# Optimization experiments

Hardware: AMD Instinct MI355X
Metric: run time of the kernel (lower is better)

Reference implementation:

```python
import jax, jax.numpy as jnp
import numpy as np

N = 50000      # nodes
DEG = 32       # avg degree
E = N * DEG + N  # edges incl. self loops
IN_DIM = 512
H = 4          # heads
D = 128        # hidden per head
SLOPE = 0.2


def setup_inputs() -> dict:
    key = jax.random.key(0)
    ks = jax.random.split(key, 12)
    features = jax.random.normal(ks[0], (N, IN_DIM), dtype=jnp.float32)
    src_r = jax.random.randint(ks[1], (N * DEG,), 0, N)
    dst_r = jax.random.randint(ks[2], (N * DEG,), 0, N)
    loop = jnp.arange(N)
    src = jnp.concatenate([src_r, loop]).astype(jnp.int32)
    dst = jnp.concatenate([dst_r, loop]).astype(jnp.int32)
    ids = jax.random.randint(ks[3], (16,), 0, N)
    s0 = 1.0 / np.sqrt(IN_DIM)
    s1 = 1.0 / np.sqrt(H * D)
    fc_w0 = jax.random.normal(ks[4], (IN_DIM, H * D), dtype=jnp.float32) * s0
    attn_l0 = jax.random.normal(ks[5], (H, D), dtype=jnp.float32) * s1
    attn_r0 = jax.random.normal(ks[6], (H, D), dtype=jnp.float32) * s1
    bias0 = jnp.zeros((H * D,), dtype=jnp.float32)
    fc_w1 = jax.random.normal(ks[7], (H * D, H * D), dtype=jnp.float32) * s1
    attn_l1 = jax.random.normal(ks[8], (H, D), dtype=jnp.float32) * s1
    attn_r1 = jax.random.normal(ks[9], (H, D), dtype=jnp.float32) * s1
    bias1 = jnp.zeros((H * D,), dtype=jnp.float32)
    return dict(features=features, fc_w0=fc_w0, attn_l0=attn_l0, attn_r0=attn_r0,
                bias0=bias0, fc_w1=fc_w1, attn_l1=attn_l1, attn_r1=attn_r1,
                bias1=bias1, src=src, dst=dst, ids=ids)


def gat_layer(h, fc_w, attn_l, attn_r, bias, src, dst, residual):
    ft = (h @ fc_w).reshape(N, H, D)                     # [N,H,D]
    el = jnp.sum(ft * attn_l, axis=-1)                   # [N,H]
    er = jnp.sum(ft * attn_r, axis=-1)                   # [N,H]
    e = jax.nn.leaky_relu(el[src] + er[dst], SLOPE)      # [E,H]
    # edge softmax over incoming edges of each dst node (self-loops guarantee coverage)
    emax = jax.ops.segment_max(e, dst, num_segments=N)   # [N,H]
    ee = jnp.exp(e - emax[dst])
    esum = jax.ops.segment_sum(ee, dst, num_segments=N)  # [N,H]
    alpha = ee / esum[dst]                               # [E,H]
    out = jax.ops.segment_sum(alpha[:, :, None] * ft[src], dst, num_segments=N)  # [N,H,D]
    if residual:
        out = out + h.reshape(N, H, D)                   # res_fc is Identity (in == H*D)
    out = out + bias.reshape(1, H, D)
    out = jax.nn.elu(out)
    return out.reshape(N, H * D)


def reference(features, fc_w0, attn_l0, attn_r0, bias0, fc_w1, attn_l1, attn_r1,
              bias1, src, dst, ids):
    h = gat_layer(features, fc_w0, attn_l0, attn_r0, bias0, src, dst, residual=False)
    h = gat_layer(h, fc_w1, attn_l1, attn_r1, bias1, src, dst, residual=True)
    h = jnp.tanh(h)
    return h[ids]  # [B, H*D] gather per id2node lookup
```

## Files before the change

kernel.cpp:

```cpp
#include <hip/hip_runtime.h>
#include <hip/hip_bf16.h>

typedef short bf16x8 __attribute__((ext_vector_type(8)));
typedef float f32x4 __attribute__((ext_vector_type(4)));

#define HD 512
#define KDIM 512
#define NHEAD 4
#define DHEAD 128
#define C1CAP 1024
#define C2CAP 16384
#define E1CAP 2048
#define E2CAP 32768
#define SCATB 64

struct PassSM {
    unsigned bm[1568];
    int2 eBuf[256];
    int fBuf[256];
    int sid[16];
    int eCnt, fCnt, eBase, fBase, s_c;
};

union PrepSM {
    PassSM pass;
    float tile[64][65];
    int s_c;
};

struct GemmSM {
    __hip_bfloat16 As[128][40];
    __hip_bfloat16 Bs[128][40];
    float pel[2][128];
    float perr[2][128];
};

__device__ int detect_bf16(const unsigned short* f, int* s_c) {
    int c = 0;
#pragma unroll
    for (int k = 0; k < 4; ++k) {
        unsigned short u = f[2 * (threadIdx.x + k * 256)];
        int e = (u >> 7) & 0xFF;
        c += (e >= 96 && e <= 140) ? 1 : 0;
    }
#pragma unroll
    for (int off = 32; off; off >>= 1) c += __shfl_xor(c, off, 64);
    if (threadIdx.x == 0) *s_c = 0;
    __syncthreads();
    if ((threadIdx.x & 63) == 0) atomicAdd(s_c, c);
    __syncthreads();
    int r = (*s_c > 512) ? 1 : 0;
    __syncthreads();
    return r;
}

template<int MODE>
__device__ void pass_scan(int pid, const int* __restrict__ src,
                          const int* __restrict__ dst, int E, int B,
                          const int* __restrict__ map1g, PassSM& sm,
                          int2* __restrict__ elist, int* ecnt, int ecap,
                          int* __restrict__ cntArr,
                          int* __restrict__ mapm, int* __restrict__ Flist,
                          int* nFr, int fcap) {
    const int t = threadIdx.x;
    const int nq = E >> 2;
    const int gid = pid * 256 + t;
    if (gid < nq) {
        const int4 d4 = ((const int4*)dst)[gid];
        const int dv[4] = {d4.x, d4.y, d4.z, d4.w};
#pragma unroll
        for (int k = 0; k < 4; ++k) {
            const int d = dv[k];
            if ((sm.bm[d >> 5] >> (d & 31)) & 1u) {
                const int e = 4 * gid + k;
                int slot;
                if (MODE == 0) {
                    slot = 0;
                    for (int q = 0; q < B; ++q) if (sm.sid[q] == d) slot = q;
                } else {
                    slot = map1g[d]; if (slot < 0) slot = 0;
                }
                int p = atomicAdd(&cntArr[slot], 1);
                int2 v; v.x = src[e]; v.y = slot | (p << (MODE == 0 ? 4 : 10));
                int pp = atomicAdd(&sm.eCnt, 1);
                if (pp < 256) sm.eBuf[pp] = v;
                else { int q = atomicAdd(ecnt, 1); if (q < ecap) elist[q] = v; }
                const int s = v.x;
                if (atomicCAS(&mapm[s], -1, -2) == -1) {
                    int q = atomicAdd(&sm.fCnt, 1);
                    if (q < 256) sm.fBuf[q] = s;
                    else {
                        int g2 = atomicAdd(nFr, 1);
                        if (g2 < fcap) { Flist[g2] = s; mapm[s] = g2; }
                        else mapm[s] = 0;
                    }
                }
            }
        }
    }
    __syncthreads();
    const int ne = (sm.eCnt < 256) ? sm.eCnt : 256;
    const int nf = (sm.fCnt < 256) ? sm.fCnt : 256;
    if (t == 0 && ne) sm.eBase = atomicAdd(ecnt, ne);
    if (t == 64 && nf) sm.fBase = atomicAdd(nFr, nf);
    __syncthreads();
    for (int i = t; i < ne; i += 256) {
        int pos = sm.eBase + i;
        if (pos < ecap) elist[pos] = sm.eBuf[i];
    }
    for (int i = t; i < nf; i += 256) {
        int q = sm.fBase + i; int s = sm.fBuf[i];
        if (q < fcap) { Flist[q] = s; mapm[s] = q; }
        else mapm[s] = 0;
    }
}

__device__ void gemm_tile(const __hip_bfloat16* __restrict__ A,
                          const __hip_bfloat16* __restrict__ Bt,
                          __hip_bfloat16* __restrict__ C,
                          const float* __restrict__ al_, const float* __restrict__ ar_,
                          float* __restrict__ el, float* __restrict__ er,
                          int cntv, int m0, int n0, GemmSM& sm) {
    const int t = threadIdx.x;
    const int lane = t & 63, wave = t >> 6;
    const int wm = (wave >> 1) * 64, wn = (wave & 1) * 64;
    const int fr = lane & 15, fk = (lane >> 4) * 8;
    const int r0 = t >> 2;
    const int c0 = (t & 3) * 8;

    int arow[2];
#pragma unroll
    for (int r = 0; r < 2; ++r) {
        int rr = m0 + r * 64 + r0;
        if (rr >= cntv) rr = cntv - 1;
        arow[r] = rr;
    }

    auto loadAB = [&](int kt, uint4 va[2], uint4 vb[2]) {
#pragma unroll
        for (int r = 0; r < 2; ++r) {
            va[r] = *(const uint4*)&A[(size_t)arow[r] * KDIM + kt + c0];
            int row = r * 64 + r0;
            vb[r] = *(const uint4*)&Bt[(size_t)(n0 + row) * KDIM + kt + c0];
        }
    };

    f32x4 acc[4][4];
#pragma unroll
    for (int i = 0; i < 4; ++i)
#pragma unroll
        for (int j = 0; j < 4; ++j)
#pragma unroll
            for (int r = 0; r < 4; ++r) acc[i][j][r] = 0.f;

    uint4 cva[2], cvb[2], nva[2], nvb[2];
    loadAB(0, cva, cvb);
    for (int kt = 0; kt < KDIM; kt += 32) {
#pragma unroll
        for (int r = 0; r < 2; ++r) {
            int row = r * 64 + r0;
            *(uint4*)&sm.As[row][c0] = cva[r];
            *(uint4*)&sm.Bs[row][c0] = cvb[r];
        }
        __syncthreads();
        if (kt + 32 < KDIM) loadAB(kt + 32, nva, nvb);
        bf16x8 af[4], bfr[4];
#pragma unroll
        for (int i = 0; i < 4; ++i) af[i]  = *(const bf16x8*)&sm.As[wm + i * 16 + fr][fk];
#pragma unroll
        for (int j = 0; j < 4; ++j) bfr[j] = *(const bf16x8*)&sm.Bs[wn + j * 16 + fr][fk];
#pragma unroll
        for (int i = 0; i < 4; ++i)
#pragma unroll
            for (int j = 0; j < 4; ++j)
                acc[i][j] = __builtin_amdgcn_mfma_f32_16x16x32_bf16(af[i], bfr[j], acc[i][j], 0, 0, 0);
        __syncthreads();
#pragma unroll
        for (int r = 0; r < 2; ++r) { cva[r] = nva[r]; cvb[r] = nvb[r]; }
    }

    const int cr = (lane >> 4) * 4;
    const int cc = lane & 15;
#pragma unroll
    for (int i = 0; i < 4; ++i)
#pragma unroll
        for (int j = 0; j < 4; ++j)
#pragma unroll
            for (int rg = 0; rg < 4; ++rg) {
                int m = m0 + wm + i * 16 + cr + rg;
                int n = n0 + wn + j * 16 + cc;
                C[(size_t)m * HD + n] = __float2bfloat16(acc[i][j][rg]);
            }

    const int h = n0 >> 7;
    float alv[4], arv[4];
#pragma unroll
    for (int j = 0; j < 4; ++j) {
        alv[j] = al_[h * DHEAD + wn + j * 16 + cc];
        arv[j] = ar_[h * DHEAD + wn + j * 16 + cc];
    }
#pragma unroll
    for (int i = 0; i < 4; ++i)
#pragma unroll
        for (int rg = 0; rg < 4; ++rg) {
            float sl = 0.f, sr = 0.f;
#pragma unroll
            for (int j = 0; j < 4; ++j) {
                float c = acc[i][j][rg];
                sl += c * alv[j];
                sr += c * arv[j];
            }
#pragma unroll
            for (int off = 1; off < 16; off <<= 1) {
                sl += __shfl_xor(sl, off, 16);
                sr += __shfl_xor(sr, off, 16);
            }
            if (cc == 0) {
                int row = wm + i * 16 + cr + rg;
                sm.pel[wn >> 6][row] = sl;
                sm.perr[wn >> 6][row] = sr;
            }
        }
    __syncthreads();
    if (t < 128) {
        int m = m0 + t;
        if (m < cntv) {
            el[m * NHEAD + h] = sm.pel[0][t] + sm.pel[1][t];
            er[m * NHEAD + h] = sm.perr[0][t] + sm.perr[1][t];
        }
    }
    __syncthreads();
}

__global__ __launch_bounds__(256) void prep_pass1_k(
    const void* __restrict__ features,
    const void* __restrict__ W0, const void* __restrict__ W1,
    __hip_bfloat16* __restrict__ Wt0, __hip_bfloat16* __restrict__ Wt1,
    const void* p0, const void* p1, const void* p2,
    const void* p3, const void* p4, const void* p5,
    float* __restrict__ smallc,
    const int* __restrict__ ids, int B, int* __restrict__ mapId,
    const int* __restrict__ src, const int* __restrict__ dst, int E,
    int2* __restrict__ E1l, int* __restrict__ counters,
    int* __restrict__ cnt1, int* __restrict__ map1, int* __restrict__ F1list) {
    __shared__ PrepSM sm;
    const int b = blockIdx.x;
    const int t = threadIdx.x;
    if (b < 128) {
        const int isbf = detect_bf16((const unsigned short*)features, &sm.s_c);
        const int mtx = b >> 6;
        const int tidx = b & 63;
        const int i0 = (tidx >> 3) * 64, j0 = (tidx & 7) * 64;
        const void* W = mtx ? W1 : W0;
        __hip_bfloat16* Wt = mtx ? Wt1 : Wt0;
        const int rr = t >> 6, cc = t & 63;
#pragma unroll
        for (int it = 0; it < 16; ++it) {
            int ii = rr + it * 4;
            size_t idx = (size_t)(i0 + ii) * 512 + j0 + cc;
            float v = isbf ? __bfloat162float(((const __hip_bfloat16*)W)[idx])
                           : ((const float*)W)[idx];
            sm.tile[ii][cc] = v;
        }
        __syncthreads();
#pragma unroll
        for (int it = 0; it < 16; ++it) {
            int jj = rr + it * 4;
            Wt[(size_t)(j0 + jj) * 512 + i0 + cc] = __float2bfloat16(sm.tile[cc][jj]);
        }
    } else if (b < 134) {
        const int isbf = detect_bf16((const unsigned short*)features, &sm.s_c);
        int which = b - 128;
        const void* p;
        switch (which) {
            case 0: p = p0; break;
            case 1: p = p1; break;
            case 2: p = p2; break;
            case 3: p = p3; break;
            case 4: p = p4; break;
            default: p = p5; break;
        }
#pragma unroll
        for (int r = 0; r < 2; ++r) {
            int e = t + r * 256;
            float v = isbf ? __bfloat162float(((const __hip_bfloat16*)p)[e])
                           : ((const float*)p)[e];
            smallc[which * 512 + e] = v;
        }
    } else if (b == 134) {
        if (t < B) atomicMax(&mapId[ids[t]], t);
    } else {
        const int pid = b - 135;
        for (int i = t; i < 1568; i += 256) sm.pass.bm[i] = 0u;
        if (t < 16) sm.pass.sid[t] = (t < B) ? ids[t] : -1;
        if (t == 0) { sm.pass.eCnt = 0; sm.pass.fCnt = 0; }
        __syncthreads();
        if (t < B) { int n = sm.pass.sid[t]; atomicOr(&sm.pass.bm[n >> 5], 1u << (n & 31)); }
        __syncthreads();
        pass_scan<0>(pid, src, dst, E, B, nullptr, sm.pass,
                     E1l, counters + 0, E1CAP, cnt1,
                     map1, F1list, counters + 2, C1CAP);
    }
}

__global__ __launch_bounds__(256) void pass2_k(
    const int* __restrict__ src, const int* __restrict__ dst, int E,
    const int* __restrict__ F1list, int* __restrict__ counters,
    const int* __restrict__ map1,
    int2* __restrict__ E2l, int* __restrict__ cnt2,
    int* __restrict__ map2, int* __restrict__ F2list) {
    __shared__ PassSM sm;
    const int t = threadIdx.x;
    for (int i = t; i < 1568; i += 256) sm.bm[i] = 0u;
    if (t == 0) { sm.eCnt = 0; sm.fCnt = 0; }
    __syncthreads();
    int nf1 = counters[2]; if (nf1 > C1CAP) nf1 = C1CAP;
    for (int i = t; i < nf1; i += 256) {
        int n = F1list[i];
        atomicOr(&sm.bm[n >> 5], 1u << (n & 31));
    }
    __syncthreads();
    pass_scan<1>(blockIdx.x, src, dst, E, 0, map1, sm,
                 E2l, counters + 1, E2CAP, cnt2,
                 map2, F2list, counters + 3, C2CAP);
}

__global__ __launch_bounds__(256) void gathscat_k(
    const void* __restrict__ feat, const int* __restrict__ F2list,
    const int* __restrict__ counters,
    const int* __restrict__ cnt1, const int* __restrict__ cnt2,
    const int2* __restrict__ E1l, const int2* __restrict__ E2l,
    const int* __restrict__ map1, const int* __restrict__ map2,
    int* __restrict__ off1, int* __restrict__ off2,
    int* __restrict__ b1, int* __restrict__ b2,
    __hip_bfloat16* __restrict__ Ac) {
    __shared__ int soff[1024];
    __shared__ int sc[256];
    __shared__ int s1[16];
    __shared__ int s_c;
    const int t = threadIdx.x;
    const int b = blockIdx.x;
    if (b < SCATB) {
        int c0 = cnt2[t * 4 + 0], c1 = cnt2[t * 4 + 1];
        int c2 = cnt2[t * 4 + 2], c3 = cnt2[t * 4 + 3];
        int tsum = c0 + c1 + c2 + c3;
        sc[t] = tsum;
        __syncthreads();
        for (int off = 1; off < 256; off <<= 1) {
            int x = (t >= off) ? sc[t - off] : 0;
            __syncthreads();
            sc[t] += x;
            __syncthreads();
        }
        int run = sc[t] - tsum;
        int b4 = t * 4;
        soff[b4 + 0] = run; run += c0;
        soff[b4 + 1] = run; run += c1;
        soff[b4 + 2] = run; run += c2;
        soff[b4 + 3] = run; run += c3;
        if (t == 0) {
            int acc = 0;
            for (int i = 0; i < 16; ++i) { s1[i] = acc; acc += cnt1[i]; }
            if (b == 0) {
                int a2 = 0;
                for (int i = 0; i < 16; ++i) { off1[i] = a2; a2 += cnt1[i]; }
                off1[16] = a2;
            }
        }
        if (b == 0) {
#pragma unroll
            for (int k = 0; k < 4; ++k) off2[b4 + k] = soff[b4 + k];
            if (t == 255) off2[1024] = run;
        }
        __syncthreads();
        int n2 = counters[1]; if (n2 > E2CAP) n2 = E2CAP;
        for (int i = b * 256 + t; i < n2; i += SCATB * 256) {
            int2 v = E2l[i];
            int y = v.y & 1023, p = v.y >> 10;
            int pos = soff[y] + p;
            int r = map2[v.x]; if (r < 0) r = 0;
            if (pos < E2CAP) b2[pos] = r;
        }
        int n1 = counters[0]; if (n1 > E1CAP) n1 = E1CAP;
        for (int i = b * 256 + t; i < n1; i += SCATB * 256) {
            int2 v = E1l[i];
            int y = v.y & 15, p = v.y >> 4;
            int pos = s1[y] + p;
            int r = map1[v.x]; if (r < 0) r = 0;
            if (pos < E1CAP) b1[pos] = r;
        }
    } else {
        const int isbf = detect_bf16((const unsigned short*)feat, &s_c);
        int cnt = counters[3]; if (cnt > C2CAP) cnt = C2CAP;
        for (int bb = b - SCATB; bb < cnt; bb += (int)gridDim.x - SCATB) {
            int row = F2list[bb];
            __hip_bfloat162 v;
            if (isbf) {
                v = *(const __hip_bfloat162*)&((const __hip_bfloat16*)feat)[(size_t)row * KDIM + t * 2];
            } else {
                const float2 f = *(const float2*)&((const float*)feat)[(size_t)row * KDIM + t * 2];
                v.x = __float2bfloat16(f.x);
                v.y = __float2bfloat16(f.y);
            }
            *(__hip_bfloat162*)&Ac[(size_t)bb * KDIM + t * 2] = v;
        }
    }
}

__global__ __launch_bounds__(256) void gemmel_k(
    const __hip_bfloat16* __restrict__ A,
    const __hip_bfloat16* __restrict__ Bt, __hip_bfloat16* __restrict__ C,
    const float* __restrict__ al_, const float* __restrict__ ar_,
    float* __restrict__ el, float* __restrict__ er,
    const int* __restrict__ countp, int cap) {
    __shared__ alignas(16) GemmSM sm;
    int cntv = *countp; if (cntv > cap) cntv = cap;
    const int nt = ((cntv + 127) >> 7) * 4;
    for (int tile = blockIdx.x; tile < nt; tile += (int)gridDim.x)
        gemm_tile(A, Bt, C, al_, ar_, el, er,
                  cntv, (tile >> 2) * 128, (tile & 3) * 128, sm);
}

__global__ __launch_bounds__(256) void agg1_k(
    const int* __restrict__ off2, const int* __restrict__ b2,
    const int* __restrict__ F1list, const int* __restrict__ map2,
    const int* __restrict__ nF1p,
    const float* __restrict__ el, const float* __restrict__ er,
    const __hip_bfloat16* __restrict__ ftc,
    const float* __restrict__ bias,
    __hip_bfloat16* __restrict__ outc) {
    int b = blockIdx.x;
    if (b >= *nF1p) return;
    int n = F1list[b];
    const int h = threadIdx.x >> 6, lane = threadIdx.x & 63;
    int rn = map2[n]; if (rn < 0) rn = 0;
    float ern = er[rn * NHEAD + h];
    int beg = off2[b], end = off2[b + 1];
    float m = -3.0e38f, l = 0.f, a0 = 0.f, a1 = 0.f;
    int i = beg;
    for (; i + 4 <= end; i += 4) {
        int r4[4]; float ev[4]; __hip_bfloat162 fv[4];
#pragma unroll
        for (int k = 0; k < 4; ++k) {
            int r = b2[i + k]; if ((unsigned)r >= C2CAP) r = 0;
            r4[k] = r;
        }
#pragma unroll
        for (int k = 0; k < 4; ++k) {
            ev[k] = el[r4[k] * NHEAD + h];
            fv[k] = *(const __hip_bfloat162*)&ftc[(size_t)r4[k] * HD + h * DHEAD + lane * 2];
        }
#pragma unroll
        for (int k = 0; k < 4; ++k) {
            float e = ev[k] + ern;
            e = (e >= 0.f) ? e : 0.2f * e;
            float mn = fmaxf(m, e);
            float sc = __expf(m - mn);
            float w  = __expf(e - mn);
            l  = l * sc + w;
            a0 = a0 * sc + w * __bfloat162float(fv[k].x);
            a1 = a1 * sc + w * __bfloat162float(fv[k].y);
            m = mn;
        }
    }
    for (; i < end; ++i) {
        int r2 = b2[i]; if ((unsigned)r2 >= C2CAP) r2 = 0;
        float e = el[r2 * NHEAD + h] + ern;
        e = (e >= 0.f) ? e : 0.2f * e;
        float mn = fmaxf(m, e);
        float sc = __expf(m - mn);
        float w  = __expf(e - mn);
        const __hip_bfloat162 f = *(const __hip_bfloat162*)&ftc[(size_t)r2 * HD + h * DHEAD + lane * 2];
        l  = l * sc + w;
        a0 = a0 * sc + w * __bfloat162float(f.x);
        a1 = a1 * sc + w * __bfloat162float(f.y);
        m = mn;
    }
    float inv = (l > 0.f) ? 1.0f / l : 0.f;
    float o0 = a0 * inv, o1 = a1 * inv;
    const float2 bb = *(const float2*)&bias[h * DHEAD + lane * 2];
    o0 += bb.x; o1 += bb.y;
    o0 = (o0 > 0.f) ? o0 : expm1f(o0);
    o1 = (o1 > 0.f) ? o1 : expm1f(o1);
    __hip_bfloat162 o2;
    o2.x = __float2bfloat16(o0);
    o2.y = __float2bfloat16(o1);
    *(__hip_bfloat162*)&outc[(size_t)b * HD + h * DHEAD + lane * 2] = o2;
}

__global__ __launch_bounds__(256) void agg2_k(
    const int* __restrict__ off1, const int* __restrict__ b1,
    const int* __restrict__ ids, const int* __restrict__ mapId,
    const int* __restrict__ map1,
    const float* __restrict__ el, const float* __restrict__ er,
    const __hip_bfloat16* __restrict__ ftc,
    const __hip_bfloat16* __restrict__ resc,
    const float* __restrict__ bias,
    void* __restrict__ out, const void* __restrict__ features) {
    __shared__ int s_c;
    const int isbf = detect_bf16((const unsigned short*)features, &s_c);
    int b = blockIdx.x;
    int n = ids[b];
    int slot = mapId[n]; if (slot < 0) slot = 0;
    const int h = threadIdx.x >> 6, lane = threadIdx.x & 63;
    int rn = map1[n]; if (rn < 0) rn = 0;
    float ern = er[rn * NHEAD + h];
    int beg = off1[slot], end = off1[slot + 1];
    float m = -3.0e38f, l = 0.f, a0 = 0.f, a1 = 0.f;
    int i = beg;
    for (; i + 4 <= end; i += 4) {
        int r4[4]; float ev[4]; __hip_bfloat162 fv[4];
#pragma unroll
        for (int k = 0; k < 4; ++k) {
            int r = b1[i + k]; if ((unsigned)r >= C1CAP) r = 0;
            r4[k] = r;
        }
#pragma unroll
        for (int k = 0; k < 4; ++k) {
            ev[k] = el[r4[k] * NHEAD + h];
            fv[k] = *(const __hip_bfloat162*)&ftc[(size_t)r4[k] * HD + h * DHEAD + lane * 2];
        }
#pragma unroll
        for (int k = 0; k < 4; ++k) {
            float e = ev[k] + ern;
            e = (e >= 0.f) ? e : 0.2f * e;
            float mn = fmaxf(m, e);
            float sc = __expf(m - mn);
            float w  = __expf(e - mn);
            l  = l * sc + w;
            a0 = a0 * sc + w * __bfloat162float(fv[k].x);
            a1 = a1 * sc + w * __bfloat162float(fv[k].y);
            m = mn;
        }
    }
    for (; i < end; ++i) {
        int r1 = b1[i]; if ((unsigned)r1 >= C1CAP) r1 = 0;
        float e = el[r1 * NHEAD + h] + ern;
        e = (e >= 0.f) ? e : 0.2f * e;
        float mn = fmaxf(m, e);
        float sc = __expf(m - mn);
        float w  = __expf(e - mn);
        const __hip_bfloat162 f = *(const __hip_bfloat162*)&ftc[(size_t)r1 * HD + h * DHEAD + lane * 2];
        l  = l * sc + w;
        a0 = a0 * sc + w * __bfloat162float(f.x);
        a1 = a1 * sc + w * __bfloat162float(f.y);
        m = mn;
    }
    float inv = (l > 0.f) ? 1.0f / l : 0.f;
    float o0 = a0 * inv, o1 = a1 * inv;
    const __hip_bfloat162 rv = *(const __hip_bfloat162*)&resc[(size_t)rn * HD + h * DHEAD + lane * 2];
    o0 += __bfloat162float(rv.x);
    o1 += __bfloat162float(rv.y);
    const float2 bb = *(const float2*)&bias[h * DHEAD + lane * 2];
    o0 += bb.x; o1 += bb.y;
    o0 = (o0 > 0.f) ? o0 : expm1f(o0);
    o1 = (o1 > 0.f) ? o1 : expm1f(o1);
    o0 = tanhf(o0);
    o1 = tanhf(o1);
    size_t oi = (size_t)b * HD + h * DHEAD + lane * 2;
    if (isbf) {
        __hip_bfloat162 o2;
        o2.x = __float2bfloat16(o0);
        o2.y = __float2bfloat16(o1);
        *(__hip_bfloat162*)&((__hip_bfloat16*)out)[oi] = o2;
    } else {
        float2 o2; o2.x = o0; o2.y = o1;
        *(float2*)&((float*)out)[oi] = o2;
    }
}

extern "C" void kernel_launch(void* const* d_in, const int* in_sizes, int n_in,
                              void* d_out, int out_size, void* d_ws, size_t ws_size,
                              hipStream_t stream) {
    const void* features = d_in[0];
    const int* src = (const int*)d_in[9];
    const int* dst = (const int*)d_in[10];
    const int* ids = (const int*)d_in[11];

    const int N = in_sizes[0] / KDIM;
    const int E = in_sizes[9];
    const int B = in_sizes[11];

    char* w = (char*)d_ws;
    auto alloc = [&](size_t bytes) {
        void* p = (void*)w;
        w += (bytes + 255) & ~(size_t)255;
        return p;
    };
    __hip_bfloat16* Wt0 = (__hip_bfloat16*)alloc(512 * 512 * 2);
    __hip_bfloat16* Wt1 = (__hip_bfloat16*)alloc(512 * 512 * 2);
    float* smallc = (float*)alloc(6 * 512 * 4);
    int* maps  = (int*)alloc((size_t)3 * N * 4);
    int* mapId = maps;
    int* map1  = maps + N;
    int* map2  = maps + 2 * N;
    int2* E1l  = (int2*)alloc((size_t)E1CAP * 8);
    int2* E2l  = (int2*)alloc((size_t)E2CAP * 8);
    int* F1list = (int*)alloc(C1CAP * 4);
    int* F2list = (int*)alloc(C2CAP * 4);
    const int zwords = 8 + 16 + 1024;
    int* zmem = (int*)alloc((size_t)zwords * 4);
    int* counters = zmem;
    int* cnt1 = zmem + 8;
    int* cnt2 = cnt1 + 16;
    int* off1 = (int*)alloc(17 * 4);
    int* off2 = (int*)alloc(1025 * 4);
    int* b1   = (int*)alloc(E1CAP * 4);
    int* b2   = (int*)alloc(E2CAP * 4);
    __hip_bfloat16* Ac   = (__hip_bfloat16*)alloc((size_t)C2CAP * KDIM * 2);
    __hip_bfloat16* ft0c = (__hip_bfloat16*)alloc((size_t)C2CAP * HD * 2);
    float* el0 = (float*)alloc((size_t)C2CAP * NHEAD * 4);
    float* er0 = (float*)alloc((size_t)C2CAP * NHEAD * 4);
    __hip_bfloat16* h1c  = (__hip_bfloat16*)alloc((size_t)C1CAP * HD * 2);
    __hip_bfloat16* ft1c = (__hip_bfloat16*)alloc((size_t)C1CAP * HD * 2);
    float* el1 = (float*)alloc((size_t)C1CAP * NHEAD * 4);
    float* er1 = (float*)alloc((size_t)C1CAP * NHEAD * 4);

    hipMemsetAsync(maps, 0xFF, (size_t)3 * N * 4, stream);
    hipMemsetAsync(zmem, 0, (size_t)zwords * 4, stream);

    float* al0c = smallc + 0 * 512;
    float* ar0c = smallc + 1 * 512;
    float* b0c  = smallc + 2 * 512;
    float* al1c = smallc + 3 * 512;
    float* ar1c = smallc + 4 * 512;
    float* b1c  = smallc + 5 * 512;

    const int nblk_scan = (E / 4 + 255) / 256;

    prep_pass1_k<<<135 + nblk_scan, 256, 0, stream>>>(
        features, d_in[1], d_in[5], Wt0, Wt1,
        d_in[2], d_in[3], d_in[4], d_in[6], d_in[7], d_in[8],
        smallc, ids, B, mapId, src, dst, E,
        E1l, counters, cnt1, map1, F1list);

    pass2_k<<<nblk_scan, 256, 0, stream>>>(src, dst, E, F1list, counters, map1,
                                           E2l, cnt2, map2, F2list);

    gathscat_k<<<2048, 256, 0, stream>>>(features, F2list, counters, cnt1, cnt2,
                                         E1l, E2l, map1, map2,
                                         off1, off2, b1, b2, Ac);

    gemmel_k<<<512, 256, 0, stream>>>(Ac, Wt0, ft0c, al0c, ar0c, el0, er0,
                                      counters + 3, C2CAP);

    agg1_k<<<C1CAP, 256, 0, stream>>>(off2, b2, F1list, map2, counters + 2,
                                      el0, er0, ft0c, b0c, h1c);

    gemmel_k<<<32, 256, 0, stream>>>(h1c, Wt1, ft1c, al1c, ar1c, el1, er1,
                                     counters + 2, C1CAP);

    agg2_k<<<B, 256, 0, stream>>>(off1, b1, ids, mapId, map1,
                                  el1, er1, ft1c, h1c, b1c,
                                  d_out, features);
}
```

Before: 332.8 us.

## Deepen GEMM prefetch, map tiles XCD-aware, and widen aggregation gather batches

The GEMM main loop now keeps two k-slices of A/B in flight in registers, double-buffering global loads against MFMA compute. Tile assignment in gemmel_k is remapped so that the four column tiles of a row panel run on blocks of the same XCD, which is meant to improve L2 reuse of the A rows. The agg1 and final aggregation loops batch 8 neighbour gathers per iteration instead of 4 to expose more memory-level parallelism. The cost is higher register pressure, and the new tile mapping assumes gridDim is a multiple of 32. If it is not, pstride could be zero or some tiles could be skipped.

Result: no change. 330.0 us (-0.8%).

```diff
diff --git a/kernel.cpp b/kernel.cpp
--- a/kernel.cpp
+++ b/kernel.cpp
@@ -153,17 +153,16 @@
 #pragma unroll
             for (int r = 0; r < 4; ++r) acc[i][j][r] = 0.f;
 
-    uint4 cva[2], cvb[2], nva[2], nvb[2];
-    loadAB(0, cva, cvb);
-    for (int kt = 0; kt < KDIM; kt += 32) {
+    auto stepStore = [&](uint4 va[2], uint4 vb[2]) {
 #pragma unroll
         for (int r = 0; r < 2; ++r) {
             int row = r * 64 + r0;
-            *(uint4*)&sm.As[row][c0] = cva[r];
-            *(uint4*)&sm.Bs[row][c0] = cvb[r];
+            *(uint4*)&sm.As[row][c0] = va[r];
+            *(uint4*)&sm.Bs[row][c0] = vb[r];
         }
         __syncthreads();
-        if (kt + 32 < KDIM) loadAB(kt + 32, nva, nvb);
+    };
+    auto stepCompute = [&]() {
         bf16x8 af[4], bfr[4];
 #pragma unroll
         for (int i = 0; i < 4; ++i) af[i]  = *(const bf16x8*)&sm.As[wm + i * 16 + fr][fk];
@@ -175,8 +174,18 @@
             for (int j = 0; j < 4; ++j)
                 acc[i][j] = __builtin_amdgcn_mfma_f32_16x16x32_bf16(af[i], bfr[j], acc[i][j], 0, 0, 0);
         __syncthreads();
-#pragma unroll
-        for (int r = 0; r < 2; ++r) { cva[r] = nva[r]; cvb[r] = nvb[r]; }
+    };
+
+    uint4 a0[2], b0[2], a1[2], b1[2];
+    loadAB(0, a0, b0);
+    loadAB(32, a1, b1);
+    for (int kt = 0; kt < KDIM; kt += 64) {
+        stepStore(a0, b0);
+        if (kt + 64 < KDIM) loadAB(kt + 64, a0, b0);
+        stepCompute();
+        stepStore(a1, b1);
+        if (kt + 96 < KDIM) loadAB(kt + 96, a1, b1);
+        stepCompute();
     }
 
     const int cr = (lane >> 4) * 4;
@@ -415,10 +424,14 @@
     const int* __restrict__ countp, int cap) {
     __shared__ alignas(16) GemmSM sm;
     int cntv = *countp; if (cntv > cap) cntv = cap;
-    const int nt = ((cntv + 127) >> 7) * 4;
-    for (int tile = blockIdx.x; tile < nt; tile += (int)gridDim.x)
-        gemm_tile(A, Bt, C, al_, ar_, el, er,
-                  cntv, (tile >> 2) * 128, (tile & 3) * 128, sm);
+    const int nP = (cntv + 127) >> 7;
+    const int xcd = blockIdx.x & 7;
+    const int s = blockIdx.x >> 3;
+    const int j = s & 3;
+    const int perXcd = (int)gridDim.x >> 3;
+    const int pstride = (perXcd >> 2) * 8;
+    for (int p = (s >> 2) * 8 + xcd; p < nP; p += pstride)
+        gemm_tile(A, Bt, C, al_, ar_, el, er, cntv, p * 128, j * 128, sm);
 }
 
 __global__ __launch_bounds__(256) void agg1_k(
@@ -438,20 +451,20 @@
     int beg = off2[b], end = off2[b + 1];
     float m = -3.0e38f, l = 0.f, a0 = 0.f, a1 = 0.f;
     int i = beg;
-    for (; i + 4 <= end; i += 4) {
-        int r4[4]; float ev[4]; __hip_bfloat162 fv[4];
-#pragma unroll
-        for (int k = 0; k < 4; ++k) {
+    for (; i + 8 <= end; i += 8) {
+        int r8[8]; float ev[8]; __hip_bfloat162 fv[8];
+#pragma unroll
+        for (int k = 0; k < 8; ++k) {
             int r = b2[i + k]; if ((unsigned)r >= C2CAP) r = 0;
-            r4[k] = r;
-        }
-#pragma unroll
-        for (int k = 0; k < 4; ++k) {
-            ev[k] = el[r4[k] * NHEAD + h];
-            fv[k] = *(const __hip_bfloat162*)&ftc[(size_t)r4[k] * HD + h * DHEAD + lane * 2];
-        }
-#pragma unroll
-        for (int k = 0; k < 4; ++k) {
+            r8[k] = r;
+        }
+#pragma unroll
+        for (int k = 0; k < 8; ++k) {
+            ev[k] = el[r8[k] * NHEAD + h];
+            fv[k] = *(const __hip_bfloat162*)&ftc[(size_t)r8[k] * HD + h * DHEAD + lane * 2];
+        }
+#pragma unroll
+        for (int k = 0; k < 8; ++k) {
             float e = ev[k] + ern;
             e = (e >= 0.f) ? e : 0.2f * e;
             float mn = fmaxf(m, e);
@@ -508,20 +521,20 @@
     int beg = off1[slot], end = off1[slot + 1];
     float m = -3.0e38f, l = 0.f, a0 = 0.f, a1 = 0.f;
     int i = beg;
-    for (; i + 4 <= end; i += 4) {
-        int r4[4]; float ev[4]; __hip_bfloat162 fv[4];
-#pragma unroll
-        for (int k = 0; k < 4; ++k) {
+    for (; i + 8 <= end; i += 8) {
+        int r8[8]; float ev[8]; __hip_bfloat162 fv[8];
+#pragma unroll
+        for (int k = 0; k < 8; ++k) {
             int r = b1[i + k]; if ((unsigned)r >= C1CAP) r = 0;
-            r4[k] = r;
-        }
-#pragma unroll
-        for (int k = 0; k < 4; ++k) {
-            ev[k] = el[r4[k] * NHEAD + h];
-            fv[k] = *(const __hip_bfloat162*)&ftc[(size_t)r4[k] * HD + h * DHEAD + lane * 2];
-        }
-#pragma unroll
-        for (int k = 0; k < 4; ++k) {
+            r8[k] = r;
+        }
+#pragma unroll
+        for (int k = 0; k < 8; ++k) {
+            ev[k] = el[r8[k] * NHEAD + h];
+            fv[k] = *(const __hip_bfloat162*)&ftc[(size_t)r8[k] * HD + h * DHEAD + lane * 2];
+        }
+#pragma unroll
+        for (int k = 0; k < 8; ++k) {
             float e = ev[k] + ern;
             e = (e >= 0.f) ? e : 0.2f * e;
             float mn = fmaxf(m, e);
```
